# Kernel tuning notes

Measured on AMD Instinct MI355X. Metric: run time of the kernel, lower is better.

## Reference

```python
import jax, jax.numpy as jnp
import numpy as np

B, T, C = 8, 1024, 768
H, D = 12, 64  # num_heads, head_size; H*D == C
BLOCK = 1024


def setup_inputs() -> dict:
    key = jax.random.key(0)
    ks = jax.random.split(key, 6)
    s = C ** -0.5  # init scale akin to torch Linear default range
    x = jax.random.normal(ks[0], (B, T, C), dtype=jnp.float32)
    Wq = jax.random.normal(ks[1], (C, H, D), dtype=jnp.float32) * s
    Wk = jax.random.normal(ks[2], (C, H, D), dtype=jnp.float32) * s
    Wv = jax.random.normal(ks[3], (C, H, D), dtype=jnp.float32) * s
    Wp = jax.random.normal(ks[4], (C, C), dtype=jnp.float32) * s
    bp = jax.random.normal(ks[5], (C,), dtype=jnp.float32) * s
    return {"x": x, "Wq": Wq, "Wk": Wk, "Wv": Wv, "Wp": Wp, "bp": bp}


def reference(x, Wq, Wk, Wv, Wp, bp):
    # Fused equivalent of the per-head loop: project all heads at once.
    q = jnp.einsum('btc,chd->bhtd', x, Wq)  # [B,H,T,D]
    k = jnp.einsum('btc,chd->bhtd', x, Wk)
    v = jnp.einsum('btc,chd->bhtd', x, Wv)
    scale = D ** -0.5
    scores = jnp.einsum('bhtd,bhsd->bhts', q, k) * scale  # [B,H,T,T]
    causal = jnp.tril(jnp.ones((T, T), dtype=bool))       # tril mask (T <= block_size)
    scores = jnp.where(causal, scores, jnp.finfo(scores.dtype).min)
    att = jax.nn.softmax(scores, axis=-1)
    # dropout layers are identity in eval mode (deterministic reference)
    out = jnp.einsum('bhts,bhsd->bhtd', att, v)            # [B,H,T,D]
    out = out.transpose(0, 2, 1, 3).reshape(B, T, H * D)   # concat heads -> [B,T,C]
    return out @ Wp.T + bp  # output projection (torch Linear: y = x W^T + b)
```

## Files before the change

### kernel.cpp

```cpp
#include <hip/hip_runtime.h>

#define BB 8
#define TT 1024
#define CC 768
#define HH 12
#define DD 64

typedef float f32x4 __attribute__((ext_vector_type(4)));
typedef short s16x8 __attribute__((ext_vector_type(8)));

__device__ __forceinline__ unsigned short f2bf(float f) {
  unsigned u = __builtin_bit_cast(unsigned, f);
  u += 0x7fffu + ((u >> 16) & 1u);
  return (unsigned short)(u >> 16);
}

#define GLOAD_LDS16(gsrc, ldst)                                                     \
  __builtin_amdgcn_global_load_lds(                                                 \
      (const __attribute__((address_space(1))) void*)(gsrc),                        \
      (__attribute__((address_space(3))) void*)(ldst), 16, 0, 0)

__global__ __launch_bounds__(256) void cast_f32_bf16(const float* __restrict__ src,
                                                     unsigned short* __restrict__ dst,
                                                     int n4) {
  int i = blockIdx.x * 256 + threadIdx.x;
  if (i >= n4) return;
  float4 v = ((const float4*)src)[i];
  ushort4 o;
  o.x = f2bf(v.x); o.y = f2bf(v.y); o.z = f2bf(v.z); o.w = f2bf(v.w);
  ((ushort4*)dst)[i] = o;
}

__global__ __launch_bounds__(256) void transpose_w(const float* __restrict__ Wq,
                                                   const float* __restrict__ Wk,
                                                   const float* __restrict__ Wv,
                                                   unsigned short* __restrict__ WT) {
  __shared__ float tile[32][33];
  int bid = blockIdx.x;
  int which = bid / (24 * 24);
  int rem = bid % (24 * 24);
  int cb = (rem / 24) * 32, nb = (rem % 24) * 32;
  const float* W = (which == 0) ? Wq : (which == 1) ? Wk : Wv;
  int t = threadIdx.x;
  int j = t & 31, i0 = t >> 5;
  #pragma unroll
  for (int rr = 0; rr < 4; ++rr) {
    int i = i0 + rr * 8;
    tile[i][j] = W[(size_t)(cb + i) * CC + nb + j];
  }
  __syncthreads();
  #pragma unroll
  for (int rr = 0; rr < 4; ++rr) {
    int i = i0 + rr * 8;
    WT[(size_t)(which * CC + nb + i) * CC + cb + j] = f2bf(tile[j][i]);
  }
}

__device__ __forceinline__ void gemm_tile(const unsigned short* __restrict__ A,
                                          const unsigned short* __restrict__ BT,
                                          int m0, int n0,
                                          unsigned short* As, unsigned short* Bs,
                                          f32x4 acc[4][4]) {
  const int t = threadIdx.x, lane = t & 63, w = t >> 6;
  const int g = lane >> 4, c = lane & 15;
  const int wr = w >> 1, wc = w & 1;
  const int srow = lane >> 3;
  const int scol = (lane & 7) * 8;
  #pragma unroll 1
  for (int kt = 0; kt < CC; kt += 64) {
    __syncthreads();
    #pragma unroll
    for (int p = 0; p < 4; ++p) {
      int row = p * 32 + w * 8 + srow;
      GLOAD_LDS16(A + (size_t)(m0 + row) * CC + kt + scol, As + (p * 32 + w * 8) * 64);
      GLOAD_LDS16(BT + (size_t)(n0 + row) * CC + kt + scol, Bs + (p * 32 + w * 8) * 64);
    }
    __syncthreads();
    #pragma unroll
    for (int ks = 0; ks < 2; ++ks) {
      s16x8 a[4], b[4];
      #pragma unroll
      for (int i = 0; i < 4; ++i) {
        a[i] = *(const s16x8*)(As + (wr * 64 + i * 16 + c) * 64 + ks * 32 + g * 8);
        b[i] = *(const s16x8*)(Bs + (wc * 64 + i * 16 + c) * 64 + ks * 32 + g * 8);
      }
      #pragma unroll
      for (int i = 0; i < 4; ++i)
        #pragma unroll
        for (int j = 0; j < 4; ++j)
          acc[i][j] = __builtin_amdgcn_mfma_f32_16x16x32_bf16(a[i], b[j], acc[i][j], 0, 0, 0);
    }
  }
}

__global__ __launch_bounds__(256) void gemm_qkv(const unsigned short* __restrict__ xb,
                                                const unsigned short* __restrict__ WT,
                                                unsigned short* __restrict__ qb,
                                                unsigned short* __restrict__ kb,
                                                unsigned short* __restrict__ vT) {
  __shared__ unsigned short As[128 * 64], Bs[128 * 64];
  int bid = blockIdx.x;
  int bm = bid % 64, bn = bid / 64;
  int m0 = bm * 128, n0 = bn * 128;
  f32x4 acc[4][4];
  #pragma unroll
  for (int i = 0; i < 4; ++i)
    #pragma unroll
    for (int j = 0; j < 4; ++j)
      acc[i][j] = (f32x4){0.f, 0.f, 0.f, 0.f};
  gemm_tile(xb, WT, m0, n0, As, Bs, acc);

  const int t = threadIdx.x, lane = t & 63, w = t >> 6;
  const int g = lane >> 4, c = lane & 15;
  const int wr = w >> 1, wc = w & 1;
  #pragma unroll
  for (int i = 0; i < 4; ++i) {
    int mrow = m0 + wr * 64 + i * 16 + g * 4;
    int b = mrow >> 10, tt_ = mrow & 1023;
    #pragma unroll
    for (int j = 0; j < 4; ++j) {
      int nbv = n0 + wc * 64 + j * 16;
      int which = nbv / CC;
      int rm = nbv - which * CC;
      int h = rm >> 6, d0 = rm & 63;
      if (which == 2) {
        ushort4 pk;
        pk.x = f2bf(acc[i][j][0]); pk.y = f2bf(acc[i][j][1]);
        pk.z = f2bf(acc[i][j][2]); pk.w = f2bf(acc[i][j][3]);
        *(ushort4*)(vT + ((size_t)(b * HH + h) * DD + d0 + c) * TT + tt_) = pk;
      } else {
        unsigned short* dst = (which ? kb : qb) +
                              ((size_t)(b * HH + h) * TT + tt_) * DD + d0 + c;
        dst[0]      = f2bf(acc[i][j][0]);
        dst[DD]     = f2bf(acc[i][j][1]);
        dst[2 * DD] = f2bf(acc[i][j][2]);
        dst[3 * DD] = f2bf(acc[i][j][3]);
      }
    }
  }
}

__global__ __launch_bounds__(256) void attn(const unsigned short* __restrict__ qb,
                                            const unsigned short* __restrict__ kb,
                                            const unsigned short* __restrict__ vT,
                                            unsigned short* __restrict__ ao) {
  __shared__ unsigned short P[4][32 * 128];
  int bid = blockIdx.x;
  int qt = bid & 7, bh = bid >> 3;
  int b = bh / HH, h = bh % HH;
  int t = threadIdx.x, lane = t & 63, w = t >> 6;
  int g = lane >> 4, c = lane & 15;
  unsigned short* Pw = P[w];
  const unsigned short* Q = qb + (size_t)bh * TT * DD;
  const unsigned short* K = kb + (size_t)bh * TT * DD;
  const unsigned short* V = vT + (size_t)bh * DD * TT;
  int q0 = qt * 128 + w * 32;

  s16x8 aq[2][2];
  #pragma unroll
  for (int mi = 0; mi < 2; ++mi)
    #pragma unroll
    for (int ks = 0; ks < 2; ++ks)
      aq[mi][ks] = *(const s16x8*)(Q + (size_t)(q0 + mi * 16 + c) * DD + ks * 32 + g * 8);

  f32x4 acco[2][4];
  float mrow[2][4], lrow[2][4];
  #pragma unroll
  for (int mi = 0; mi < 2; ++mi) {
    #pragma unroll
    for (int nj = 0; nj < 4; ++nj) acco[mi][nj] = (f32x4){0.f, 0.f, 0.f, 0.f};
    #pragma unroll
    for (int r = 0; r < 4; ++r) { mrow[mi][r] = -1e30f; lrow[mi][r] = 0.f; }
  }
  const float scale2 = 0.18033688011112042f;

  for (int kt = 0; kt <= qt; ++kt) {
    int s0 = kt * 128;
    f32x4 accs[2][8];
    #pragma unroll
    for (int mi = 0; mi < 2; ++mi)
      #pragma unroll
      for (int nj = 0; nj < 8; ++nj) accs[mi][nj] = (f32x4){0.f, 0.f, 0.f, 0.f};

    #pragma unroll
    for (int ks = 0; ks < 2; ++ks) {
      s16x8 bk[8];
      #pragma unroll
      for (int nj = 0; nj < 8; ++nj)
        bk[nj] = *(const s16x8*)(K + (size_t)(s0 + nj * 16 + c) * DD + ks * 32 + g * 8);
      #pragma unroll
      for (int mi = 0; mi < 2; ++mi)
        #pragma unroll
        for (int nj = 0; nj < 8; ++nj)
          accs[mi][nj] = __builtin_amdgcn_mfma_f32_16x16x32_bf16(aq[mi][ks], bk[nj],
                                                                 accs[mi][nj], 0, 0, 0);
    }

    bool diag = (kt == qt);
    #pragma unroll
    for (int mi = 0; mi < 2; ++mi) {
      float nm[4], fs[4];
      #pragma unroll
      for (int r = 0; r < 4; ++r) {
        int trow = q0 + mi * 16 + g * 4 + r;
        #pragma unroll
        for (int nj = 0; nj < 8; ++nj) {
          float v = accs[mi][nj][r] * scale2;
          if (diag && (s0 + nj * 16 + c) > trow) v = -1e30f;
          accs[mi][nj][r] = v;
        }
        float mx = accs[mi][0][r];
        #pragma unroll
        for (int nj = 1; nj < 8; ++nj) mx = fmaxf(mx, accs[mi][nj][r]);
        mx = fmaxf(mx, __shfl_xor(mx, 1));
        mx = fmaxf(mx, __shfl_xor(mx, 2));
        mx = fmaxf(mx, __shfl_xor(mx, 4));
        mx = fmaxf(mx, __shfl_xor(mx, 8));
        float newm = fmaxf(mrow[mi][r], mx);
        fs[r] = __builtin_amdgcn_exp2f(mrow[mi][r] - newm);
        mrow[mi][r] = newm;
        nm[r] = newm;
      }
      #pragma unroll
      for (int nj = 0; nj < 8; ++nj)
        #pragma unroll
        for (int r = 0; r < 4; ++r)
          accs[mi][nj][r] = __builtin_amdgcn_exp2f(accs[mi][nj][r] - nm[r]);
      #pragma unroll
      for (int r = 0; r < 4; ++r) {
        float s = 0.f;
        #pragma unroll
        for (int nj = 0; nj < 8; ++nj) s += accs[mi][nj][r];
        s += __shfl_xor(s, 1);
        s += __shfl_xor(s, 2);
        s += __shfl_xor(s, 4);
        s += __shfl_xor(s, 8);
        lrow[mi][r] = lrow[mi][r] * fs[r] + s;
      }
      #pragma unroll
      for (int nj = 0; nj < 4; ++nj)
        #pragma unroll
        for (int r = 0; r < 4; ++r) acco[mi][nj][r] *= fs[r];
      #pragma unroll
      for (int nj = 0; nj < 8; ++nj)
        #pragma unroll
        for (int r = 0; r < 4; ++r) {
          int tr = mi * 16 + g * 4 + r;
          Pw[(tr * 128 + nj * 16 + c) ^ ((tr & 7) << 3)] = f2bf(accs[mi][nj][r]);
        }
    }
    asm volatile("" ::: "memory");

    #pragma unroll
    for (int ks = 0; ks < 4; ++ks) {
      s16x8 bv[4];
      #pragma unroll
      for (int nj = 0; nj < 4; ++nj)
        bv[nj] = *(const s16x8*)(V + (size_t)(nj * 16 + c) * TT + s0 + ks * 32 + g * 8);
      #pragma unroll
      for (int mi = 0; mi < 2; ++mi) {
        int tr = mi * 16 + c;
        s16x8 pa = *(const s16x8*)(Pw + ((tr * 128 + ks * 32 + g * 8) ^ ((tr & 7) << 3)));
        #pragma unroll
        for (int nj = 0; nj < 4; ++nj)
          acco[mi][nj] = __builtin_amdgcn_mfma_f32_16x16x32_bf16(pa, bv[nj],
                                                                 acco[mi][nj], 0, 0, 0);
      }
    }
    asm volatile("" ::: "memory");
  }

  #pragma unroll
  for (int mi = 0; mi < 2; ++mi)
    #pragma unroll
    for (int r = 0; r < 4; ++r) {
      float inv = 1.0f / lrow[mi][r];
      int trow = q0 + mi * 16 + g * 4 + r;
      size_t rowb = ((size_t)b * TT + trow) * CC + h * DD;
      #pragma unroll
      for (int nj = 0; nj < 4; ++nj)
        ao[rowb + nj * 16 + c] = f2bf(acco[mi][nj][r] * inv);
    }
}

__global__ __launch_bounds__(256) void gemm_proj(const unsigned short* __restrict__ ao,
                                                 const unsigned short* __restrict__ WpB,
                                                 const float* __restrict__ bp,
                                                 float* __restrict__ out) {
  __shared__ unsigned short As[128 * 64], Bs[128 * 64];
  int bid = blockIdx.x;
  int bm = bid % 64, bn = bid / 64;
  int m0 = bm * 128, n0 = bn * 128;
  f32x4 acc[4][4];
  #pragma unroll
  for (int i = 0; i < 4; ++i)
    #pragma unroll
    for (int j = 0; j < 4; ++j)
      acc[i][j] = (f32x4){0.f, 0.f, 0.f, 0.f};
  gemm_tile(ao, WpB, m0, n0, As, Bs, acc);

  const int t = threadIdx.x, lane = t & 63, w = t >> 6;
  const int g = lane >> 4, c = lane & 15;
  const int wr = w >> 1, wc = w & 1;
  #pragma unroll
  for (int i = 0; i < 4; ++i) {
    int mrow = m0 + wr * 64 + i * 16 + g * 4;
    #pragma unroll
    for (int j = 0; j < 4; ++j) {
      int nn = n0 + wc * 64 + j * 16 + c;
      float bias = bp[nn];
      float* dst = out + (size_t)mrow * CC + nn;
      dst[0]        = acc[i][j][0] + bias;
      dst[CC]       = acc[i][j][1] + bias;
      dst[2 * CC]   = acc[i][j][2] + bias;
      dst[3 * CC]   = acc[i][j][3] + bias;
    }
  }
}

extern "C" void kernel_launch(void* const* d_in, const int* in_sizes, int n_in,
                              void* d_out, int out_size, void* d_ws, size_t ws_size,
                              hipStream_t stream) {
  (void)in_sizes; (void)n_in; (void)out_size; (void)ws_size;
  const float* x  = (const float*)d_in[0];
  const float* Wq = (const float*)d_in[1];
  const float* Wk = (const float*)d_in[2];
  const float* Wv = (const float*)d_in[3];
  const float* Wp = (const float*)d_in[4];
  const float* bp = (const float*)d_in[5];
  float* out = (float*)d_out;

  char* ws = (char*)d_ws;
  unsigned short* xb  = (unsigned short*)(ws);
  unsigned short* WT  = (unsigned short*)(ws + 12582912);
  unsigned short* WpB = (unsigned short*)(ws + 16121856);
  unsigned short* qb  = (unsigned short*)(ws + 17301504);
  unsigned short* kb  = (unsigned short*)(ws + 29884416);
  unsigned short* vT  = (unsigned short*)(ws + 42467328);
  unsigned short* aob = (unsigned short*)(ws + 55050240);

  cast_f32_bf16<<<6144, 256, 0, stream>>>(x, xb, 1572864);
  cast_f32_bf16<<<576, 256, 0, stream>>>(Wp, WpB, 147456);
  transpose_w<<<1728, 256, 0, stream>>>(Wq, Wk, Wv, WT);
  gemm_qkv<<<1152, 256, 0, stream>>>(xb, WT, qb, kb, vT);
  attn<<<768, 256, 0, stream>>>(qb, kb, vT, aob);
  gemm_proj<<<384, 256, 0, stream>>>(aob, WpB, bp, out);
}
```

Measured before the change: 315.8 us.

## Rebalance causal attention with paired 16-row strips and fold scale into Q

The attention kernel now has each wave process two 16-row query strips, p and 63-p, so causal work is evenly balanced across waves and blocks. The previous design used 32-row tiles indexed by block, which gave later blocks far more KV tiles. KV tiles shrink to 64 columns with finer diagonal trimming, and the softmax scale (with log2e) is folded into Q at projection time, removing a multiply per score. Smaller per-wave state plus launch_bounds(256,4) aim for higher occupancy, at the cost of less K/V register reuse per load and storing Q in bf16 after scaling.

```diff
diff --git a/kernel.cpp b/kernel.cpp
--- a/kernel.cpp
+++ b/kernel.cpp
@@ -8,6 +8,8 @@
 
 typedef float f32x4 __attribute__((ext_vector_type(4)));
 typedef short s16x8 __attribute__((ext_vector_type(8)));
+
+#define SCALE2 0.18033688011112042f
 
 __device__ __forceinline__ unsigned short f2bf(float f) {
   unsigned u = __builtin_bit_cast(unsigned, f);
@@ -129,24 +131,25 @@
         pk.z = f2bf(acc[i][j][2]); pk.w = f2bf(acc[i][j][3]);
         *(ushort4*)(vT + ((size_t)(b * HH + h) * DD + d0 + c) * TT + tt_) = pk;
       } else {
+        float sc = which ? 1.0f : SCALE2;
         unsigned short* dst = (which ? kb : qb) +
                               ((size_t)(b * HH + h) * TT + tt_) * DD + d0 + c;
-        dst[0]      = f2bf(acc[i][j][0]);
-        dst[DD]     = f2bf(acc[i][j][1]);
-        dst[2 * DD] = f2bf(acc[i][j][2]);
-        dst[3 * DD] = f2bf(acc[i][j][3]);
-      }
-    }
-  }
-}
-
-__global__ __launch_bounds__(256) void attn(const unsigned short* __restrict__ qb,
-                                            const unsigned short* __restrict__ kb,
-                                            const unsigned short* __restrict__ vT,
-                                            unsigned short* __restrict__ ao) {
-  __shared__ unsigned short P[4][32 * 128];
+        dst[0]      = f2bf(acc[i][j][0] * sc);
+        dst[DD]     = f2bf(acc[i][j][1] * sc);
+        dst[2 * DD] = f2bf(acc[i][j][2] * sc);
+        dst[3 * DD] = f2bf(acc[i][j][3] * sc);
+      }
+    }
+  }
+}
+
+__global__ __launch_bounds__(256, 4) void attn(const unsigned short* __restrict__ qb,
+                                               const unsigned short* __restrict__ kb,
+                                               const unsigned short* __restrict__ vT,
+                                               unsigned short* __restrict__ ao) {
+  __shared__ unsigned short P[4][16 * 64];
   int bid = blockIdx.x;
-  int qt = bid & 7, bh = bid >> 3;
+  int sub = bid & 7, bh = bid >> 3;
   int b = bh / HH, h = bh % HH;
   int t = threadIdx.x, lane = t & 63, w = t >> 6;
   int g = lane >> 4, c = lane & 15;
@@ -154,133 +157,121 @@
   const unsigned short* Q = qb + (size_t)bh * TT * DD;
   const unsigned short* K = kb + (size_t)bh * TT * DD;
   const unsigned short* V = vT + (size_t)bh * DD * TT;
-  int q0 = qt * 128 + w * 32;
-
-  s16x8 aq[2][2];
-  #pragma unroll
-  for (int mi = 0; mi < 2; ++mi)
+  int p = sub * 4 + w;
+
+  #pragma unroll 1
+  for (int half = 0; half < 2; ++half) {
+    int strip = half ? (63 - p) : p;
+    int q0 = strip * 16;
+
+    s16x8 aq[2];
     #pragma unroll
     for (int ks = 0; ks < 2; ++ks)
-      aq[mi][ks] = *(const s16x8*)(Q + (size_t)(q0 + mi * 16 + c) * DD + ks * 32 + g * 8);
-
-  f32x4 acco[2][4];
-  float mrow[2][4], lrow[2][4];
-  #pragma unroll
-  for (int mi = 0; mi < 2; ++mi) {
-    #pragma unroll
-    for (int nj = 0; nj < 4; ++nj) acco[mi][nj] = (f32x4){0.f, 0.f, 0.f, 0.f};
-    #pragma unroll
-    for (int r = 0; r < 4; ++r) { mrow[mi][r] = -1e30f; lrow[mi][r] = 0.f; }
-  }
-  const float scale2 = 0.18033688011112042f;
-
-  for (int kt = 0; kt <= qt; ++kt) {
-    int s0 = kt * 128;
-    f32x4 accs[2][8];
-    #pragma unroll
-    for (int mi = 0; mi < 2; ++mi)
-      #pragma unroll
-      for (int nj = 0; nj < 8; ++nj) accs[mi][nj] = (f32x4){0.f, 0.f, 0.f, 0.f};
-
-    #pragma unroll
-    for (int ks = 0; ks < 2; ++ks) {
-      s16x8 bk[8];
-      #pragma unroll
-      for (int nj = 0; nj < 8; ++nj)
-        bk[nj] = *(const s16x8*)(K + (size_t)(s0 + nj * 16 + c) * DD + ks * 32 + g * 8);
-      #pragma unroll
-      for (int mi = 0; mi < 2; ++mi)
-        #pragma unroll
-        for (int nj = 0; nj < 8; ++nj)
-          accs[mi][nj] = __builtin_amdgcn_mfma_f32_16x16x32_bf16(aq[mi][ks], bk[nj],
-                                                                 accs[mi][nj], 0, 0, 0);
-    }
-
-    bool diag = (kt == qt);
-    #pragma unroll
-    for (int mi = 0; mi < 2; ++mi) {
+      aq[ks] = *(const s16x8*)(Q + (size_t)(q0 + c) * DD + ks * 32 + g * 8);
+
+    f32x4 acco[4];
+    float mrow[4], lrow[4];
+    #pragma unroll
+    for (int nj = 0; nj < 4; ++nj) acco[nj] = (f32x4){0.f, 0.f, 0.f, 0.f};
+    #pragma unroll
+    for (int r = 0; r < 4; ++r) { mrow[r] = -1e30f; lrow[r] = 0.f; }
+
+    int ntile = (q0 + 79) >> 6;
+    #pragma unroll 1
+    for (int kt = 0; kt < ntile; ++kt) {
+      int s0 = kt * 64;
+      f32x4 accs[4];
+      #pragma unroll
+      for (int nj = 0; nj < 4; ++nj) accs[nj] = (f32x4){0.f, 0.f, 0.f, 0.f};
+
+      #pragma unroll
+      for (int ks = 0; ks < 2; ++ks) {
+        s16x8 bk[4];
+        #pragma unroll
+        for (int nj = 0; nj < 4; ++nj)
+          bk[nj] = *(const s16x8*)(K + (size_t)(s0 + nj * 16 + c) * DD + ks * 32 + g * 8);
+        #pragma unroll
+        for (int nj = 0; nj < 4; ++nj)
+          accs[nj] = __builtin_amdgcn_mfma_f32_16x16x32_bf16(aq[ks], bk[nj],
+                                                             accs[nj], 0, 0, 0);
+      }
+
       float nm[4], fs[4];
+      bool diag = (kt == ntile - 1);
+      if (diag) {
+        #pragma unroll
+        for (int r = 0; r < 4; ++r) {
+          int trow = q0 + g * 4 + r;
+          #pragma unroll
+          for (int nj = 0; nj < 4; ++nj)
+            if (s0 + nj * 16 + c > trow) accs[nj][r] = -1e30f;
+        }
+      }
       #pragma unroll
       for (int r = 0; r < 4; ++r) {
-        int trow = q0 + mi * 16 + g * 4 + r;
-        #pragma unroll
-        for (int nj = 0; nj < 8; ++nj) {
-          float v = accs[mi][nj][r] * scale2;
-          if (diag && (s0 + nj * 16 + c) > trow) v = -1e30f;
-          accs[mi][nj][r] = v;
-        }
-        float mx = accs[mi][0][r];
-        #pragma unroll
-        for (int nj = 1; nj < 8; ++nj) mx = fmaxf(mx, accs[mi][nj][r]);
+        float mx = fmaxf(fmaxf(accs[0][r], accs[1][r]), fmaxf(accs[2][r], accs[3][r]));
         mx = fmaxf(mx, __shfl_xor(mx, 1));
         mx = fmaxf(mx, __shfl_xor(mx, 2));
         mx = fmaxf(mx, __shfl_xor(mx, 4));
         mx = fmaxf(mx, __shfl_xor(mx, 8));
-        float newm = fmaxf(mrow[mi][r], mx);
-        fs[r] = __builtin_amdgcn_exp2f(mrow[mi][r] - newm);
-        mrow[mi][r] = newm;
+        float newm = fmaxf(mrow[r], mx);
+        fs[r] = __builtin_amdgcn_exp2f(mrow[r] - newm);
+        mrow[r] = newm;
         nm[r] = newm;
       }
       #pragma unroll
-      for (int nj = 0; nj < 8; ++nj)
+      for (int nj = 0; nj < 4; ++nj)
         #pragma unroll
         for (int r = 0; r < 4; ++r)
-          accs[mi][nj][r] = __builtin_amdgcn_exp2f(accs[mi][nj][r] - nm[r]);
+          accs[nj][r] = __builtin_amdgcn_exp2f(accs[nj][r] - nm[r]);
       #pragma unroll
       for (int r = 0; r < 4; ++r) {
-        float s = 0.f;
-        #pragma unroll
-        for (int nj = 0; nj < 8; ++nj) s += accs[mi][nj][r];
+        float s = (accs[0][r] + accs[1][r]) + (accs[2][r] + accs[3][r]);
         s += __shfl_xor(s, 1);
         s += __shfl_xor(s, 2);
         s += __shfl_xor(s, 4);
         s += __shfl_xor(s, 8);
-        lrow[mi][r] = lrow[mi][r] * fs[r] + s;
+        lrow[r] = lrow[r] * fs[r] + s;
       }
       #pragma unroll
       for (int nj = 0; nj < 4; ++nj)
         #pragma unroll
-        for (int r = 0; r < 4; ++r) acco[mi][nj][r] *= fs[r];
-      #pragma unroll
-      for (int nj = 0; nj < 8; ++nj)
+        for (int r = 0; r < 4; ++r) acco[nj][r] *= fs[r];
+
+      #pragma unroll
+      for (int nj = 0; nj < 4; ++nj)
         #pragma unroll
         for (int r = 0; r < 4; ++r) {
-          int tr = mi * 16 + g * 4 + r;
-          Pw[(tr * 128 + nj * 16 + c) ^ ((tr & 7) << 3)] = f2bf(accs[mi][nj][r]);
+          int tr = g * 4 + r;
+          Pw[(tr * 64 + nj * 16 + c) ^ ((tr & 7) << 3)] = f2bf(accs[nj][r]);
         }
-    }
-    asm volatile("" ::: "memory");
-
-    #pragma unroll
-    for (int ks = 0; ks < 4; ++ks) {
-      s16x8 bv[4];
+      asm volatile("" ::: "memory");
+
+      #pragma unroll
+      for (int ks = 0; ks < 2; ++ks) {
+        s16x8 bv[4];
+        #pragma unroll
+        for (int nj = 0; nj < 4; ++nj)
+          bv[nj] = *(const s16x8*)(V + (size_t)(nj * 16 + c) * TT + s0 + ks * 32 + g * 8);
+        s16x8 pa = *(const s16x8*)(Pw + ((c * 64 + ks * 32 + g * 8) ^ ((c & 7) << 3)));
+        #pragma unroll
+        for (int nj = 0; nj < 4; ++nj)
+          acco[nj] = __builtin_amdgcn_mfma_f32_16x16x32_bf16(pa, bv[nj],
+                                                             acco[nj], 0, 0, 0);
+      }
+      asm volatile("" ::: "memory");
+    }
+
+    #pragma unroll
+    for (int r = 0; r < 4; ++r) {
+      float inv = 1.0f / lrow[r];
+      int trow = q0 + g * 4 + r;
+      size_t rowb = ((size_t)b * TT + trow) * CC + h * DD;
       #pragma unroll
       for (int nj = 0; nj < 4; ++nj)
-        bv[nj] = *(const s16x8*)(V + (size_t)(nj * 16 + c) * TT + s0 + ks * 32 + g * 8);
-      #pragma unroll
-      for (int mi = 0; mi < 2; ++mi) {
-        int tr = mi * 16 + c;
-        s16x8 pa = *(const s16x8*)(Pw + ((tr * 128 + ks * 32 + g * 8) ^ ((tr & 7) << 3)));
-        #pragma unroll
-        for (int nj = 0; nj < 4; ++nj)
-          acco[mi][nj] = __builtin_amdgcn_mfma_f32_16x16x32_bf16(pa, bv[nj],
-                                                                 acco[mi][nj], 0, 0, 0);
-      }
-    }
-    asm volatile("" ::: "memory");
-  }
-
-  #pragma unroll
-  for (int mi = 0; mi < 2; ++mi)
-    #pragma unroll
-    for (int r = 0; r < 4; ++r) {
-      float inv = 1.0f / lrow[mi][r];
-      int trow = q0 + mi * 16 + g * 4 + r;
-      size_t rowb = ((size_t)b * TT + trow) * CC + h * DD;
-      #pragma unroll
-      for (int nj = 0; nj < 4; ++nj)
-        ao[rowb + nj * 16 + c] = f2bf(acco[mi][nj][r] * inv);
-    }
+        ao[rowb + nj * 16 + c] = f2bf(acco[nj][r] * inv);
+    }
+  }
 }
 
 __global__ __launch_bounds__(256) void gemm_proj(const unsigned short* __restrict__ ao,
```

Result: faster. 286.5 us (-9.3%).
